# Kernel tuning notes

Measured on AMD Instinct MI355X. Metric: run time of the kernel, lower is better.

Reference implementation:

```python
import jax, jax.numpy as jnp
import numpy as np

# SudokuUniqueHVBox with type='h': depthwise (1,9) sum conv over width,
# NNCompare(.,1), nearest-upsample back, min with mask, 1x1 conv (all -1, bias 1)
# + relu collapsing channels, then Or with uniq mask, And with input mask.


def setup_inputs() -> dict:
    key = jax.random.key(0)
    mask = jax.random.randint(key, (65536, 9, 9, 9), 0, 2).astype(jnp.float32)
    return {"mask": mask}


def reference(mask: jnp.ndarray) -> jnp.ndarray:
    # mask: [B, C=9, H=9, W=9]
    # depthwise sum conv kernel (1,9): sum over width -> [B,9,9,1]
    s = jnp.sum(mask, axis=3, keepdims=True)
    # NNCompare(s, 1) = min(relu(s - 1 + 1), relu(1 + 1 - s))
    uniq_down = jnp.minimum(jax.nn.relu(s), jax.nn.relu(2.0 - s))  # [B,9,9,1]
    # nearest upsample scale (1,9): broadcast over width
    uniq = jnp.broadcast_to(uniq_down, mask.shape)  # [B,9,9,9]
    not_uniq = jnp.minimum(uniq, mask)
    # 1x1 conv: weight all -1 over 9 channels, bias 1, then ReLU -> [B,1,9,9]
    cell = jax.nn.relu(1.0 - jnp.sum(not_uniq, axis=1, keepdims=True))
    merged = jnp.clip(jnp.maximum(jnp.broadcast_to(cell, mask.shape), uniq), 0.0, 1.0)
    return jnp.clip(jnp.minimum(mask, merged), 0.0, 1.0)
```

## Files before the change

kernel.cpp:

```cpp
#include <hip/hip_runtime.h>


typedef float f4 __attribute__((ext_vector_type(4)));

#define BPB 4
#define FPB (BPB * 729)
#define NF4 (FPB / 4)
#define ROWS (BPB * 81)

__global__ __launch_bounds__(256, 8) void sudoku_hbox_kernel(
    const float* __restrict__ in, float* __restrict__ out, int B) {
    __shared__ unsigned rowbits[ROWS + 8];

    const int tid = threadIdx.x;
    const long long base = (long long)blockIdx.x * FPB;
    const f4* gin = (const f4*)(in + base);
    f4* gout = (f4*)(out + base);

    if (tid < ROWS + 8 - 256) rowbits[tid + 256] = 0u;
    rowbits[tid] = 0u;
    __syncthreads();

    #pragma unroll
    for (int i = 0; i < 3; ++i) {
        int idx = tid + i * 256;
        if (idx < NF4) {
            f4 v = gin[idx];
            int o  = idx * 4;
            int r0 = o / 9;
            int w0 = o - r0 * 9;
            unsigned m4 = (v.x > 0.5f ? 1u : 0u) | (v.y > 0.5f ? 2u : 0u) |
                          (v.z > 0.5f ? 4u : 0u) | (v.w > 0.5f ? 8u : 0u);
            unsigned or0 = (m4 << w0) & 0x1FFu;
            atomicOr(&rowbits[r0], or0);
            if (w0 > 5) {
                unsigned or1 = m4 >> (9 - w0);
                atomicOr(&rowbits[r0 + 1], or1);
            }
        }
    }
    __syncthreads();

    if (tid < BPB * 9) {
        const int bl = tid / 9;
        const int h  = tid - bl * 9;
        const int rb = bl * 81 + h;
        unsigned rows[9], uniqm = 0;
        #pragma unroll
        for (int c = 0; c < 9; ++c) {
            rows[c] = rowbits[rb + c * 9];
            if (__popc(rows[c]) == 1) uniqm |= (1u << c);
        }
        unsigned covered = 0;
        #pragma unroll
        for (int c = 0; c < 9; ++c)
            covered |= ((uniqm >> c) & 1u) ? rows[c] : 0u;
        #pragma unroll
        for (int c = 0; c < 9; ++c) {
            unsigned ob = ((uniqm >> c) & 1u) ? rows[c] : (rows[c] & ~covered);
            rowbits[rb + c * 9] = ob;
        }
    }
    __syncthreads();

    #pragma unroll
    for (int i = 0; i < 3; ++i) {
        int idx = tid + i * 256;
        if (idx < NF4) {
            int o  = idx * 4;
            int r0 = o / 9;
            int w0 = o - r0 * 9;
            unsigned v0 = rowbits[r0];
            unsigned v1 = rowbits[r0 + 1];
            unsigned win = (v0 >> w0) | (v1 << (9 - w0));
            f4 ov;
            ov.x = (win & 1u) ? 1.0f : 0.0f;
            ov.y = (win & 2u) ? 1.0f : 0.0f;
            ov.z = (win & 4u) ? 1.0f : 0.0f;
            ov.w = (win & 8u) ? 1.0f : 0.0f;
            __builtin_nontemporal_store(ov, &gout[idx]);
        }
    }
}

extern "C" void kernel_launch(void* const* d_in, const int* in_sizes, int n_in,
                              void* d_out, int out_size, void* d_ws, size_t ws_size,
                              hipStream_t stream) {
    const float* in = (const float*)d_in[0];
    float* out = (float*)d_out;
    const int total = in_sizes[0];
    const int B = total / 729;
    const int nblk = (B + BPB - 1) / BPB;
    hipLaunchKernelGGL(sudoku_hbox_kernel, dim3(nblk), dim3(256), 0, stream,
                       in, out, B);
}
```

Baseline: 61.35 us.

## Give each wave its own boards and replace block barriers with wave-local fences

Each wavefront now handles 4 boards on its own, so __syncthreads is replaced by an lgkmcnt wait plus scheduler barriers inside the wave. LDS atomicOr row accumulation is dropped: per-float4 4-bit masks go into a byte array and row bits are rebuilt from three bytes. All 12 loads per lane are issued before any processing to raise memory-level parallelism. This costs more registers (launch bounds drop to 4 blocks per CU), and correctness depends on DS operations being ordered within a wave.

Result: no change. 62.04 us (+1.1%).

```diff
diff --git a/kernel.cpp b/kernel.cpp
--- a/kernel.cpp
+++ b/kernel.cpp
@@ -3,52 +3,62 @@
 
 typedef float f4 __attribute__((ext_vector_type(4)));
 
-#define BPB 4
-#define FPB (BPB * 729)
-#define NF4 (FPB / 4)
-#define ROWS (BPB * 81)
+#define WAVES 4
+#define BPW 4
+#define NF4W 729
+#define ROWSW 324
 
-__global__ __launch_bounds__(256, 8) void sudoku_hbox_kernel(
+#define WAVE_FENCE() do {                                   \
+    __builtin_amdgcn_sched_barrier(0);                      \
+    asm volatile("s_waitcnt lgkmcnt(0)" ::: "memory");      \
+    __builtin_amdgcn_sched_barrier(0);                      \
+} while (0)
+
+__global__ __launch_bounds__(256, 4) void sudoku_hbox_kernel(
     const float* __restrict__ in, float* __restrict__ out, int B) {
-    __shared__ unsigned rowbits[ROWS + 8];
+    __shared__ unsigned char m4s[WAVES][736];
+    __shared__ unsigned rowb[WAVES][ROWSW + 2];
 
-    const int tid = threadIdx.x;
-    const long long base = (long long)blockIdx.x * FPB;
-    const f4* gin = (const f4*)(in + base);
-    f4* gout = (f4*)(out + base);
+    const int tid  = threadIdx.x;
+    const int w    = tid >> 6;
+    const int lane = tid & 63;
+    const long long wbase4 = ((long long)blockIdx.x * WAVES + w) * NF4W;
+    const f4* gin  = (const f4*)in + wbase4;
+    f4* gout       = (f4*)out + wbase4;
+    unsigned char* my4  = m4s[w];
+    unsigned*      myrow = rowb[w];
 
-    if (tid < ROWS + 8 - 256) rowbits[tid + 256] = 0u;
-    rowbits[tid] = 0u;
-    __syncthreads();
-
+    f4 v[12];
     #pragma unroll
-    for (int i = 0; i < 3; ++i) {
-        int idx = tid + i * 256;
-        if (idx < NF4) {
-            f4 v = gin[idx];
-            int o  = idx * 4;
-            int r0 = o / 9;
-            int w0 = o - r0 * 9;
-            unsigned m4 = (v.x > 0.5f ? 1u : 0u) | (v.y > 0.5f ? 2u : 0u) |
-                          (v.z > 0.5f ? 4u : 0u) | (v.w > 0.5f ? 8u : 0u);
-            unsigned or0 = (m4 << w0) & 0x1FFu;
-            atomicOr(&rowbits[r0], or0);
-            if (w0 > 5) {
-                unsigned or1 = m4 >> (9 - w0);
-                atomicOr(&rowbits[r0 + 1], or1);
-            }
+    for (int i = 0; i < 12; ++i) {
+        int idx = lane + 64 * i;
+        if (idx < NF4W) v[i] = gin[idx];
+    }
+    #pragma unroll
+    for (int i = 0; i < 12; ++i) {
+        int idx = lane + 64 * i;
+        if (idx < NF4W) {
+            unsigned m = (v[i].x > 0.5f ? 1u : 0u) | (v[i].y > 0.5f ? 2u : 0u) |
+                         (v[i].z > 0.5f ? 4u : 0u) | (v[i].w > 0.5f ? 8u : 0u);
+            my4[idx] = (unsigned char)m;
         }
     }
-    __syncthreads();
+    WAVE_FENCE();
 
-    if (tid < BPB * 9) {
-        const int bl = tid / 9;
-        const int h  = tid - bl * 9;
-        const int rb = bl * 81 + h;
+    if (lane < BPW * 9) {
+        const int bl = lane / 9;
+        const int h  = lane - bl * 9;
         unsigned rows[9], uniqm = 0;
         #pragma unroll
         for (int c = 0; c < 9; ++c) {
-            rows[c] = rowbits[rb + c * 9];
+            int r  = bl * 81 + c * 9 + h;
+            int f0 = 9 * r;
+            int a  = f0 & 3;
+            int j0 = f0 >> 2;
+            unsigned win = ((unsigned)my4[j0] >> a) |
+                           ((unsigned)my4[j0 + 1] << (4 - a)) |
+                           ((unsigned)my4[j0 + 2] << (8 - a));
+            rows[c] = win & 0x1FFu;
             if (__popc(rows[c]) == 1) uniqm |= (1u << c);
         }
         unsigned covered = 0;
@@ -58,20 +68,20 @@
         #pragma unroll
         for (int c = 0; c < 9; ++c) {
             unsigned ob = ((uniqm >> c) & 1u) ? rows[c] : (rows[c] & ~covered);
-            rowbits[rb + c * 9] = ob;
+            myrow[bl * 81 + c * 9 + h] = ob;
         }
     }
-    __syncthreads();
+    WAVE_FENCE();
 
     #pragma unroll
-    for (int i = 0; i < 3; ++i) {
-        int idx = tid + i * 256;
-        if (idx < NF4) {
+    for (int i = 0; i < 12; ++i) {
+        int idx = lane + 64 * i;
+        if (idx < NF4W) {
             int o  = idx * 4;
             int r0 = o / 9;
             int w0 = o - r0 * 9;
-            unsigned v0 = rowbits[r0];
-            unsigned v1 = rowbits[r0 + 1];
+            unsigned v0 = myrow[r0];
+            unsigned v1 = myrow[r0 + 1];
             unsigned win = (v0 >> w0) | (v1 << (9 - w0));
             f4 ov;
             ov.x = (win & 1u) ? 1.0f : 0.0f;
@@ -90,7 +100,7 @@
     float* out = (float*)d_out;
     const int total = in_sizes[0];
     const int B = total / 729;
-    const int nblk = (B + BPB - 1) / BPB;
+    const int nblk = (B + WAVES * BPW - 1) / (WAVES * BPW);
     hipLaunchKernelGGL(sudoku_hbox_kernel, dim3(nblk), dim3(256), 0, stream,
                        in, out, B);
 }
```
